# Kernel optimization log

Measured on AMD Instinct MI355X. Metric: run time of the kernel, lower is better.

## Reference

```python
import jax, jax.numpy as jnp
import numpy as np

DIM = 1024
HEADS = 16
HEAD_DIM = 64
INNER = HEADS * HEAD_DIM  # 1024
B, N = 4, 2048
EPS = 1e-5


def setup_inputs() -> dict:
    key = jax.random.key(0)
    ks = jax.random.split(key, 5)
    x = jax.random.normal(ks[0], (B, N, DIM), dtype=jnp.float32)
    w_qkv = jax.random.normal(ks[1], (DIM, 3 * INNER), dtype=jnp.float32) * (DIM ** -0.5)
    w_out = jax.random.normal(ks[2], (INNER, DIM), dtype=jnp.float32) * (INNER ** -0.5)
    b_out = jax.random.normal(ks[3], (DIM,), dtype=jnp.float32) * 0.01
    ln_gamma = jnp.ones((DIM,), dtype=jnp.float32)
    ln_beta = jnp.zeros((DIM,), dtype=jnp.float32)
    return {"x": x, "w_qkv": w_qkv, "w_out": w_out, "b_out": b_out,
            "ln_gamma": ln_gamma, "ln_beta": ln_beta}


def reference(x, w_qkv, w_out, b_out, ln_gamma, ln_beta):
    scale = HEAD_DIM ** -0.5
    qkv = x @ w_qkv  # [b, n, 3*inner]
    q, k, v = jnp.split(qkv, 3, axis=-1)
    q = q * scale
    # [b, n, h*d] -> [b, h, n, d]
    def to_heads(t):
        b, n, _ = t.shape
        return t.reshape(b, n, HEADS, HEAD_DIM).transpose(0, 2, 1, 3)
    q, k, v = to_heads(q), to_heads(k), to_heads(v)
    scores = jnp.einsum('bhid,bhjd->bhij', q, k)
    attn = jax.nn.softmax(scores, axis=-1)  # max-subtraction (detached) is internal
    out = jnp.einsum('bhij,bhjd->bhid', attn, v)
    out = out.transpose(0, 2, 1, 3).reshape(x.shape[0], x.shape[1], INNER)
    out = out @ w_out + b_out
    # LayerNorm over last dim
    mu = out.mean(axis=-1, keepdims=True)
    var = out.var(axis=-1, keepdims=True)
    out = (out - mu) * jax.lax.rsqrt(var + EPS)
    return out * ln_gamma + ln_beta
```

## Files before the change

kernel.cpp:

```cpp
#include <hip/hip_runtime.h>


typedef __bf16 bf16;
typedef __bf16 bf16x4 __attribute__((ext_vector_type(4)));
typedef __bf16 bf16x8 __attribute__((ext_vector_type(8)));
typedef float f32x4 __attribute__((ext_vector_type(4)));
typedef float f32x16 __attribute__((ext_vector_type(16)));
typedef unsigned int u32x2 __attribute__((ext_vector_type(2)));
typedef unsigned int u32x4 __attribute__((ext_vector_type(4)));

#define QSCALE_LOG2E 0.18033688011112042f

#define GLOAD_LDS16(gp, lp)                                                   \
  __builtin_amdgcn_global_load_lds(                                           \
      (const __attribute__((address_space(1))) unsigned int*)(const void*)(gp), \
      (__attribute__((address_space(3))) unsigned int*)(void*)(lp), 16, 0, 0)

__device__ __forceinline__ float fexp2(float x) {
#if __has_builtin(__builtin_amdgcn_exp2f)
  return __builtin_amdgcn_exp2f(x);
#else
  return __expf(x * 0.6931471805599453f);
#endif
}

__device__ __forceinline__ unsigned pack2t(float lo, float hi) {
  return __builtin_amdgcn_perm(__float_as_uint(hi), __float_as_uint(lo), 0x07060302u);
}

__global__ __launch_bounds__(256) void cvt_k(const float* __restrict__ in,
                                             bf16* __restrict__ out) {
  const size_t i = ((size_t)blockIdx.x * 256 + threadIdx.x) * 8;
  float4 a = *(const float4*)(in + i);
  float4 b = *(const float4*)(in + i + 4);
  bf16x8 o = {(bf16)a.x, (bf16)a.y, (bf16)a.z, (bf16)a.w,
              (bf16)b.x, (bf16)b.y, (bf16)b.z, (bf16)b.w};
  *(bf16x8*)(out + i) = o;
}

__global__ __launch_bounds__(256) void transpose_k(const float* __restrict__ in,
                                                   bf16* __restrict__ out,
                                                   int Kd, int Nd) {
  __shared__ bf16 t[32][36];
  const int n0 = blockIdx.x * 32, k0 = blockIdx.y * 32;
  const int r = threadIdx.x >> 3, c4 = (threadIdx.x & 7) * 4;
  float4 v = *(const float4*)(in + (size_t)(k0 + r) * Nd + n0 + c4);
  t[c4 + 0][r] = (bf16)v.x; t[c4 + 1][r] = (bf16)v.y;
  t[c4 + 2][r] = (bf16)v.z; t[c4 + 3][r] = (bf16)v.w;
  __syncthreads();
  bf16x4 o = *(const bf16x4*)&t[r][c4];
  *(bf16x4*)(out + (size_t)(n0 + r) * Kd + k0 + c4) = o;
}

template <bool QKV>
__global__ __launch_bounds__(256) void gemm2(const bf16* __restrict__ A,
                                             const bf16* __restrict__ Bt,
                                             bf16* __restrict__ C,
                                             bf16* __restrict__ Vt) {
  __shared__ bf16 As[128][32];
  __shared__ bf16 Bs[128][32];
  const int tid = threadIdx.x;
  const int l = tid & 63, w = tid >> 6;
  const int g = l >> 4, q = l & 15;
  const int wm = w >> 1, wn = w & 1;
  const int m0 = blockIdx.x * 128, n0 = blockIdx.y * 128;
  const int lr = l >> 2, lc = (l & 3) * 8;

  f32x4 acc[4][4] = {};

  for (int k0 = 0; k0 < 1024; k0 += 32) {
    __syncthreads();
#pragma unroll
    for (int i = 0; i < 2; i++) {
      const int c = w + i * 4;
      GLOAD_LDS16(A + (size_t)(m0 + c * 16 + lr) * 1024 + k0 + lc, &As[c * 16][0]);
      GLOAD_LDS16(Bt + (size_t)(n0 + c * 16 + lr) * 1024 + k0 + lc, &Bs[c * 16][0]);
    }
    __syncthreads();

    bf16x8 af[4], bfr[4];
#pragma unroll
    for (int mi = 0; mi < 4; mi++)
      af[mi] = *(const bf16x8*)&As[wm * 64 + mi * 16 + q][g * 8];
#pragma unroll
    for (int ni = 0; ni < 4; ni++)
      bfr[ni] = *(const bf16x8*)&Bs[wn * 64 + ni * 16 + q][g * 8];
#pragma unroll
    for (int mi = 0; mi < 4; mi++)
#pragma unroll
      for (int ni = 0; ni < 4; ni++)
        acc[mi][ni] = __builtin_amdgcn_mfma_f32_16x16x32_bf16(af[mi], bfr[ni], acc[mi][ni], 0, 0, 0);
  }

  if (QKV && n0 >= 2048) {
#pragma unroll
    for (int mi = 0; mi < 4; mi++)
#pragma unroll
      for (int ni = 0; ni < 4; ni++) {
        const int vcol = n0 - 2048 + wn * 64 + ni * 16 + q;
        const int h = vcol >> 6, d = vcol & 63;
        const int t0 = m0 + wm * 64 + mi * 16 + g * 4;
        const int b = t0 >> 11, n = t0 & 2047;
        bf16x4 o = {(bf16)acc[mi][ni][0], (bf16)acc[mi][ni][1],
                    (bf16)acc[mi][ni][2], (bf16)acc[mi][ni][3]};
        *(bf16x4*)(Vt + ((size_t)(b * 16 + h) * 64 + d) * 2048 + n) = o;
      }
  } else {
    const int ldc = QKV ? 2048 : 1024;
    const float s = (QKV && n0 < 1024) ? QSCALE_LOG2E : 1.0f;
#pragma unroll
    for (int mi = 0; mi < 4; mi++)
#pragma unroll
      for (int ni = 0; ni < 4; ni++) {
        const int col = n0 + wn * 64 + ni * 16 + q;
#pragma unroll
        for (int r = 0; r < 4; r++) {
          const int row = m0 + wm * 64 + mi * 16 + g * 4 + r;
          C[(size_t)row * ldc + col] = (bf16)(acc[mi][ni][r] * s);
        }
      }
  }
}

__global__ __launch_bounds__(256) void attn_k(const bf16* __restrict__ qk,
                                              const bf16* __restrict__ vt,
                                              bf16* __restrict__ aout) {
  __shared__ bf16 Ks[2][64][64];
  __shared__ bf16 Vs[2][64][64];
  const int tid = threadIdx.x;
  const int l = tid & 63, w = tid >> 6;
  const int q = l & 31, hi = l >> 5, q7 = q & 7;
  const int h = blockIdx.y, b = blockIdx.z;
  const int qbase = blockIdx.x * 128 + w * 32;

  const bf16* Kg = qk + (size_t)(b * 2048) * 2048 + 1024 + h * 64;
  const bf16* Vg = vt + ((size_t)(b * 16 + h) * 64) * 2048;

  bf16x8 qf[4];
  {
    const bf16* Qr = qk + (size_t)(b * 2048 + qbase + q) * 2048 + h * 64 + hi * 8;
#pragma unroll
    for (int i = 0; i < 4; i++) qf[i] = *(const bf16x8*)(Qr + i * 16);
  }
  const bf16 one = (bf16)1.0f;
  const bf16x8 onesf = {one, one, one, one, one, one, one, one};

  const int r0 = tid >> 3, sp0 = ((tid & 7) ^ (r0 & 7)) * 8;
  const int ub = (tid >> 6) << 9;
#define STAGE_KV(buf, kt)                                                       \
  do {                                                                          \
    GLOAD_LDS16(Kg + (size_t)((kt) + r0) * 2048 + sp0, &Ks[buf][0][0] + ub);    \
    GLOAD_LDS16(Vg + (size_t)r0 * 2048 + (kt) + sp0, &Vs[buf][0][0] + ub);      \
    GLOAD_LDS16(Kg + (size_t)((kt) + 32 + r0) * 2048 + sp0,                     \
                &Ks[buf][0][0] + 2048 + ub);                                    \
    GLOAD_LDS16(Vg + (size_t)(32 + r0) * 2048 + (kt) + sp0,                     \
                &Vs[buf][0][0] + 2048 + ub);                                    \
  } while (0)

  float m = -1e30f;
  f32x16 oacc[2] = {};
  f32x16 lacc = {};

  STAGE_KV(0, 0);
  __syncthreads();
  int cur = 0;

  for (int kt = 0; kt < 2048; kt += 64) {
    if (kt + 64 < 2048) STAGE_KV(cur ^ 1, kt + 64);

    const char* Kb = (const char*)&Ks[cur][0][0];
    const char* Vb = (const char*)&Vs[cur][0][0];

    f32x16 st[2];
    __builtin_amdgcn_s_setprio(1);
#pragma unroll
    for (int s = 0; s < 2; s++) {
      f32x16 acc = {};
#pragma unroll
      for (int i = 0; i < 4; i++) {
        bf16x8 kf = *(const bf16x8*)(Kb + (s * 32 + q) * 128 + (((2 * i + hi) ^ q7) << 4));
        acc = __builtin_amdgcn_mfma_f32_32x32x16_bf16(kf, qf[i], acc, 0, 0, 0);
      }
      st[s] = acc;
    }
    __builtin_amdgcn_s_setprio(0);

    bf16x8 vfr[2][4];
#pragma unroll
    for (int dblk = 0; dblk < 2; dblk++)
#pragma unroll
      for (int t = 0; t < 4; t++)
        vfr[dblk][t] = *(const bf16x8*)(Vb + (dblk * 32 + q) * 128 + (((2 * t + hi) ^ q7) << 4));

    float mx[8];
#pragma unroll
    for (int r = 0; r < 8; r++)
      mx[r] = fmaxf(fmaxf(st[0][r], st[0][r + 8]), fmaxf(st[1][r], st[1][r + 8]));
#pragma unroll
    for (int o = 4; o > 0; o >>= 1)
#pragma unroll
      for (int r = 0; r < o; r++) mx[r] = fmaxf(mx[r], mx[r + o]);
    float tmax;
    {
      u32x2 t2 = __builtin_amdgcn_permlane32_swap(__float_as_uint(mx[0]),
                                                  __float_as_uint(mx[0]), false, false);
      tmax = fmaxf(__uint_as_float(t2[0]), __uint_as_float(t2[1]));
    }
    if (__ballot(tmax > m)) {
      const float mnew = fmaxf(m, tmax);
      const float corr = fexp2(m - mnew);
      m = mnew;
#pragma unroll
      for (int dblk = 0; dblk < 2; dblk++)
#pragma unroll
        for (int r = 0; r < 16; r++) oacc[dblk][r] *= corr;
      lacc[0] *= corr;
    }
#pragma unroll
    for (int s = 0; s < 2; s++)
#pragma unroll
      for (int r = 0; r < 16; r++) st[s][r] = fexp2(st[s][r] - m);

    bf16x8 pfrag[4];
#pragma unroll
    for (int s = 0; s < 2; s++)
#pragma unroll
      for (int ks = 0; ks < 2; ks++) {
        const unsigned a0 = pack2t(st[s][8 * ks + 0], st[s][8 * ks + 1]);
        const unsigned a1 = pack2t(st[s][8 * ks + 2], st[s][8 * ks + 3]);
        const unsigned b0 = pack2t(st[s][8 * ks + 4], st[s][8 * ks + 5]);
        const unsigned b1 = pack2t(st[s][8 * ks + 6], st[s][8 * ks + 7]);
        u32x2 w0 = __builtin_amdgcn_permlane32_swap(a0, b0, false, false);
        u32x2 w1 = __builtin_amdgcn_permlane32_swap(a1, b1, false, false);
        u32x4 bw = {w0[0], w1[0], w0[1], w1[1]};
        pfrag[2 * s + ks] = __builtin_bit_cast(bf16x8, bw);
      }

    __builtin_amdgcn_s_setprio(1);
#pragma unroll
    for (int dblk = 0; dblk < 2; dblk++)
#pragma unroll
      for (int t = 0; t < 4; t++)
        oacc[dblk] = __builtin_amdgcn_mfma_f32_32x32x16_bf16(vfr[dblk][t], pfrag[t],
                                                             oacc[dblk], 0, 0, 0);
#pragma unroll
    for (int t = 0; t < 4; t++)
      lacc = __builtin_amdgcn_mfma_f32_32x32x16_bf16(onesf, pfrag[t], lacc, 0, 0, 0);
    __builtin_amdgcn_s_setprio(0);

    __syncthreads();
    cur ^= 1;
  }

  const float inv = 1.f / lacc[0];
  bf16* orow = aout + (size_t)(b * 2048 + qbase + q) * 1024 + h * 64 + hi * 4;
#pragma unroll
  for (int dblk = 0; dblk < 2; dblk++)
#pragma unroll
    for (int rg = 0; rg < 4; rg++) {
      bf16x4 o = {(bf16)(oacc[dblk][4 * rg + 0] * inv), (bf16)(oacc[dblk][4 * rg + 1] * inv),
                  (bf16)(oacc[dblk][4 * rg + 2] * inv), (bf16)(oacc[dblk][4 * rg + 3] * inv)};
      *(bf16x4*)(orow + dblk * 32 + rg * 8) = o;
    }
#undef STAGE_KV
}

__global__ __launch_bounds__(256) void ln_k(const bf16* __restrict__ proj,
                                            const float* __restrict__ bo,
                                            const float* __restrict__ gam,
                                            const float* __restrict__ bet,
                                            float* __restrict__ out) {
  const int row = blockIdx.x, tid = threadIdx.x;
  const int l = tid & 63, w = tid >> 6;
  bf16x4 pv = *(const bf16x4*)(proj + (size_t)row * 1024 + tid * 4);
  float4 bv = *(const float4*)(bo + tid * 4);
  float v0 = (float)pv[0] + bv.x, v1 = (float)pv[1] + bv.y;
  float v2 = (float)pv[2] + bv.z, v3 = (float)pv[3] + bv.w;
  float s = v0 + v1 + v2 + v3;
  float ss = v0 * v0 + v1 * v1 + v2 * v2 + v3 * v3;
#pragma unroll
  for (int off = 32; off > 0; off >>= 1) {
    s += __shfl_xor(s, off);
    ss += __shfl_xor(ss, off);
  }
  __shared__ float red[8];
  if (l == 0) { red[w] = s; red[w + 4] = ss; }
  __syncthreads();
  const float S = red[0] + red[1] + red[2] + red[3];
  const float SS = red[4] + red[5] + red[6] + red[7];
  const float mean = S * (1.f / 1024.f);
  const float var = SS * (1.f / 1024.f) - mean * mean;
  const float rs = rsqrtf(var + 1e-5f);
  float4 gv = *(const float4*)(gam + tid * 4);
  float4 btv = *(const float4*)(bet + tid * 4);
  float4 o;
  o.x = (v0 - mean) * rs * gv.x + btv.x;
  o.y = (v1 - mean) * rs * gv.y + btv.y;
  o.z = (v2 - mean) * rs * gv.z + btv.z;
  o.w = (v3 - mean) * rs * gv.w + btv.w;
  *(float4*)(out + (size_t)row * 1024 + tid * 4) = o;
}

extern "C" void kernel_launch(void* const* d_in, const int* in_sizes, int n_in,
                              void* d_out, int out_size, void* d_ws, size_t ws_size,
                              hipStream_t stream) {
  const float* x      = (const float*)d_in[0];
  const float* w_qkv  = (const float*)d_in[1];
  const float* w_out  = (const float*)d_in[2];
  const float* b_out  = (const float*)d_in[3];
  const float* gamma  = (const float*)d_in[4];
  const float* beta   = (const float*)d_in[5];
  float* out = (float*)d_out;

  char* ws = (char*)d_ws;
  bf16* xbf   = (bf16*)(ws);
  bf16* wqkvT = (bf16*)(ws + 16777216);
  bf16* woutT = (bf16*)(ws + 23068672);
  bf16* qkbuf = (bf16*)(ws + 25165824);
  bf16* vt    = (bf16*)(ws + 58720256);
  bf16* aout  = xbf;
  bf16* proj  = vt;

  dim3 blk(256);
  cvt_k<<<4096, blk, 0, stream>>>(x, xbf);
  transpose_k<<<dim3(96, 32), blk, 0, stream>>>(w_qkv, wqkvT, 1024, 3072);
  transpose_k<<<dim3(32, 32), blk, 0, stream>>>(w_out, woutT, 1024, 1024);
  gemm2<true><<<dim3(64, 24), blk, 0, stream>>>(xbf, wqkvT, qkbuf, vt);
  attn_k<<<dim3(16, 16, 4), blk, 0, stream>>>(qkbuf, vt, aout);
  gemm2<false><<<dim3(64, 8), blk, 0, stream>>>(aout, woutT, proj, nullptr);
  ln_k<<<8192, blk, 0, stream>>>(proj, b_out, gamma, beta, out);
}
```

Baseline: 242.2 us.

## Triple-buffer attention K/V staging, swizzle grid, compute row sums on VALU

The attention kernel now uses three LDS buffers for K/V tiles and prefetches two tiles ahead. The old double-buffer plus trailing __syncthreads is replaced by explicit vmcnt waits and a single barrier per iteration. The softmax denominator moves from an extra ones-vector MFMA to a VALU sum with a permlane swap, and the launch becomes a flat 1D grid remapped so that blocks sharing a head across XCDs are grouped. The goal is to hide load latency and trim MFMA work and synchronisation, at the cost of more LDS (48KB per block) and some risk that the hand-written waitcnt ordering is subtly wrong.

```diff
diff --git a/kernel.cpp b/kernel.cpp
--- a/kernel.cpp
+++ b/kernel.cpp
@@ -122,16 +122,20 @@
   }
 }
 
-__global__ __launch_bounds__(256) void attn_k(const bf16* __restrict__ qk,
-                                              const bf16* __restrict__ vt,
-                                              bf16* __restrict__ aout) {
-  __shared__ bf16 Ks[2][64][64];
-  __shared__ bf16 Vs[2][64][64];
+__global__ __launch_bounds__(256, 3) void attn_k(const bf16* __restrict__ qk,
+                                                 const bf16* __restrict__ vt,
+                                                 bf16* __restrict__ aout) {
+  __shared__ bf16 Ks[3][64][64];
+  __shared__ bf16 Vs[3][64][64];
   const int tid = threadIdx.x;
   const int l = tid & 63, w = tid >> 6;
   const int q = l & 31, hi = l >> 5, q7 = q & 7;
-  const int h = blockIdx.y, b = blockIdx.z;
-  const int qbase = blockIdx.x * 128 + w * 32;
+
+  const int flat = blockIdx.x;
+  const int logical = (flat & 7) * 128 + (flat >> 3);
+  const int qt = logical & 15, bh = logical >> 4;
+  const int h = bh & 15, b = bh >> 4;
+  const int qbase = qt * 128 + w * 32;
 
   const bf16* Kg = qk + (size_t)(b * 2048) * 2048 + 1024 + h * 64;
   const bf16* Vg = vt + ((size_t)(b * 16 + h) * 64) * 2048;
@@ -142,31 +146,36 @@
 #pragma unroll
     for (int i = 0; i < 4; i++) qf[i] = *(const bf16x8*)(Qr + i * 16);
   }
-  const bf16 one = (bf16)1.0f;
-  const bf16x8 onesf = {one, one, one, one, one, one, one, one};
 
   const int r0 = tid >> 3, sp0 = ((tid & 7) ^ (r0 & 7)) * 8;
   const int ub = (tid >> 6) << 9;
 #define STAGE_KV(buf, kt)                                                       \
   do {                                                                          \
-    GLOAD_LDS16(Kg + (size_t)((kt) + r0) * 2048 + sp0, &Ks[buf][0][0] + ub);    \
-    GLOAD_LDS16(Vg + (size_t)r0 * 2048 + (kt) + sp0, &Vs[buf][0][0] + ub);      \
-    GLOAD_LDS16(Kg + (size_t)((kt) + 32 + r0) * 2048 + sp0,                     \
-                &Ks[buf][0][0] + 2048 + ub);                                    \
-    GLOAD_LDS16(Vg + (size_t)(32 + r0) * 2048 + (kt) + sp0,                     \
-                &Vs[buf][0][0] + 2048 + ub);                                    \
+    bf16* kd = &Ks[buf][0][0];                                                  \
+    bf16* vd = &Vs[buf][0][0];                                                  \
+    GLOAD_LDS16(Kg + (size_t)((kt) + r0) * 2048 + sp0, kd + ub);                \
+    GLOAD_LDS16(Vg + (size_t)r0 * 2048 + (kt) + sp0, vd + ub);                  \
+    GLOAD_LDS16(Kg + (size_t)((kt) + 32 + r0) * 2048 + sp0, kd + 2048 + ub);    \
+    GLOAD_LDS16(Vg + (size_t)(32 + r0) * 2048 + (kt) + sp0, vd + 2048 + ub);    \
   } while (0)
 
-  float m = -1e30f;
+  float m = -1e30f, lsum = 0.f;
   f32x16 oacc[2] = {};
-  f32x16 lacc = {};
 
   STAGE_KV(0, 0);
-  __syncthreads();
-  int cur = 0;
+  STAGE_KV(1, 64);
+  int cur = 0, nxt2 = 2;
 
   for (int kt = 0; kt < 2048; kt += 64) {
-    if (kt + 64 < 2048) STAGE_KV(cur ^ 1, kt + 64);
+    if (kt == 2048 - 64) {
+      asm volatile("s_waitcnt vmcnt(0)" ::: "memory");
+    } else {
+      asm volatile("s_waitcnt vmcnt(4)" ::: "memory");
+    }
+    __builtin_amdgcn_sched_barrier(0);
+    __builtin_amdgcn_s_barrier();
+
+    if (kt + 128 < 2048) STAGE_KV(nxt2, kt + 128);
 
     const char* Kb = (const char*)&Ks[cur][0][0];
     const char* Vb = (const char*)&Vs[cur][0][0];
@@ -206,20 +215,27 @@
                                                   __float_as_uint(mx[0]), false, false);
       tmax = fmaxf(__uint_as_float(t2[0]), __uint_as_float(t2[1]));
     }
+    float corr = 1.0f;
     if (__ballot(tmax > m)) {
       const float mnew = fmaxf(m, tmax);
-      const float corr = fexp2(m - mnew);
+      corr = fexp2(m - mnew);
       m = mnew;
 #pragma unroll
       for (int dblk = 0; dblk < 2; dblk++)
 #pragma unroll
         for (int r = 0; r < 16; r++) oacc[dblk][r] *= corr;
-      lacc[0] *= corr;
-    }
+    }
+    float tsum = 0.f;
 #pragma unroll
     for (int s = 0; s < 2; s++)
 #pragma unroll
-      for (int r = 0; r < 16; r++) st[s][r] = fexp2(st[s][r] - m);
+      for (int r = 0; r < 16; r++) { st[s][r] = fexp2(st[s][r] - m); tsum += st[s][r]; }
+    {
+      u32x2 t2 = __builtin_amdgcn_permlane32_swap(__float_as_uint(tsum),
+                                                  __float_as_uint(tsum), false, false);
+      tsum = __uint_as_float(t2[0]) + __uint_as_float(t2[1]);
+    }
+    lsum = lsum * corr + tsum;
 
     bf16x8 pfrag[4];
 #pragma unroll
@@ -243,16 +259,13 @@
       for (int t = 0; t < 4; t++)
         oacc[dblk] = __builtin_amdgcn_mfma_f32_32x32x16_bf16(vfr[dblk][t], pfrag[t],
                                                              oacc[dblk], 0, 0, 0);
-#pragma unroll
-    for (int t = 0; t < 4; t++)
-      lacc = __builtin_amdgcn_mfma_f32_32x32x16_bf16(onesf, pfrag[t], lacc, 0, 0, 0);
     __builtin_amdgcn_s_setprio(0);
 
-    __syncthreads();
-    cur ^= 1;
-  }
-
-  const float inv = 1.f / lacc[0];
+    cur = (cur == 2) ? 0 : cur + 1;
+    nxt2 = (nxt2 == 2) ? 0 : nxt2 + 1;
+  }
+
+  const float inv = 1.f / lsum;
   bf16* orow = aout + (size_t)(b * 2048 + qbase + q) * 1024 + h * 64 + hi * 4;
 #pragma unroll
   for (int dblk = 0; dblk < 2; dblk++)
@@ -326,7 +339,7 @@
   transpose_k<<<dim3(96, 32), blk, 0, stream>>>(w_qkv, wqkvT, 1024, 3072);
   transpose_k<<<dim3(32, 32), blk, 0, stream>>>(w_out, woutT, 1024, 1024);
   gemm2<true><<<dim3(64, 24), blk, 0, stream>>>(xbf, wqkvT, qkbuf, vt);
-  attn_k<<<dim3(16, 16, 4), blk, 0, stream>>>(qkbuf, vt, aout);
+  attn_k<<<1024, blk, 0, stream>>>(qkbuf, vt, aout);
   gemm2<false><<<dim3(64, 8), blk, 0, stream>>>(aout, woutT, proj, nullptr);
   ln_k<<<8192, blk, 0, stream>>>(proj, b_out, gamma, beta, out);
 }
```

Result: faster. 218.9 us (-9.6%).
